# Kernel tuning notes

Measured on AMD Instinct MI355X. Metric: run time of the kernel, lower is better.

The kernel has to match this reference:

```python
import jax, jax.numpy as jnp
import numpy as np

E = 8          # num_experts
K = 2          # top_k
D = 1024       # hidden_size
I = 4096       # intermediate_size
AUX_COEF = 0.02


def setup_inputs() -> dict:
    key = jax.random.key(0)
    ks = jax.random.split(key, 5)
    x = jax.random.normal(ks[0], (4, 2048, D), dtype=jnp.float32)
    w_gate = jax.random.normal(ks[1], (E, D), dtype=jnp.float32) * 0.02   # router, nn.Linear weight [E, D]
    wg = jax.random.normal(ks[2], (E, D, I), dtype=jnp.float32) * 0.02    # gate_proj per expert
    wu = jax.random.normal(ks[3], (E, D, I), dtype=jnp.float32) * 0.02    # up_proj per expert
    wd = jax.random.normal(ks[4], (E, I, D), dtype=jnp.float32) * 0.02    # down_proj per expert
    return {"x": x, "w_gate": w_gate, "wg": wg, "wu": wu, "wd": wd}


def reference(x, w_gate, wg, wu, wd):
    B, T, Dm = x.shape
    xf = x.reshape(-1, Dm)                                   # [N, D]
    N = xf.shape[0]

    # 1) Router: softmax (in fp32) + top-k, renormalize top-k weights
    logits = xf @ w_gate.T                                   # [N, E]
    probs = jax.nn.softmax(logits.astype(jnp.float32), axis=-1)
    topk_w, topk_idx = jax.lax.top_k(probs, K)               # [N, K]
    topk_w = (topk_w / topk_w.sum(-1, keepdims=True)).astype(x.dtype)

    # Per-expert combine weight (zero when expert not selected) — math-equivalent
    # to the original gather/scatter-add loop but jit-friendly and vectorized.
    onehot = jax.nn.one_hot(topk_idx, E, dtype=x.dtype)      # [N, K, E]
    combine = jnp.einsum('nk,nke->ne', topk_w, onehot)       # [N, E]

    # 2) Experts: SwiGLU FFN, combined with routing weights
    out = jnp.zeros_like(xf)
    for e in range(E):  # fixed small loop over structurally distinct experts
        h = jax.nn.silu(xf @ wg[e]) * (xf @ wu[e])           # [N, I]
        out = out + combine[:, e:e + 1] * (h @ wd[e])        # [N, D]

    # 3) Load-balancing aux loss (Switch Transformer)
    f = onehot.sum((0, 1)).astype(jnp.float32) / (N * K)     # dispatch fraction per expert
    p = probs.mean(0)                                        # mean routing prob per expert
    aux_loss = AUX_COEF * E * jnp.sum(f * p)

    return out.reshape(B, T, Dm), aux_loss
```

## Files before the change

### kernel.cpp

```cpp
#include <hip/hip_runtime.h>
#include <hip/hip_bf16.h>
#include <cstdint>
#include <cstddef>

#define NE 8
#define TK 2
#define DM 1024
#define IM 4096
#define NT 8192
#define NS (NT*TK)
#define SCAP (NS+256)
#define MAXT 72

typedef __bf16 bf16_t;
typedef __bf16 bf16x8 __attribute__((ext_vector_type(8)));
typedef __bf16 bf16x4 __attribute__((ext_vector_type(4)));
typedef float f32x4 __attribute__((ext_vector_type(4)));

__device__ __forceinline__ void async_cp16(const bf16_t* g, bf16_t* l) {
  __builtin_amdgcn_global_load_lds(
      (__attribute__((address_space(1))) void*)(const_cast<bf16_t*>(g)),
      (__attribute__((address_space(3))) void*)(l), 16, 0, 0);
}

__global__ void transpose_cvt(const float* __restrict__ src, bf16_t* __restrict__ dst,
                              int R, int C) {
  __shared__ float t[32][33];
  int bx = blockIdx.x * 32, by = blockIdx.y * 32;
  size_t zb = (size_t)blockIdx.z * R * C;
  int tx = threadIdx.x, ty = threadIdx.y;
#pragma unroll
  for (int i = 0; i < 4; ++i)
    t[ty + i*8][tx] = src[zb + (size_t)(by + ty + i*8) * C + bx + tx];
  __syncthreads();
#pragma unroll
  for (int i = 0; i < 4; ++i)
    dst[zb + (size_t)(bx + ty + i*8) * R + by + tx] = (bf16_t)t[tx][ty + i*8];
}

__global__ void pack_gu(const float* __restrict__ wg, const float* __restrict__ wu,
                        bf16_t* __restrict__ Wgu) {
  __shared__ float t[32][33];
  int sel = blockIdx.z & 1, e = blockIdx.z >> 1;
  const float* src = sel ? wu : wg;
  size_t zb = (size_t)e * DM * IM;
  int bx = blockIdx.x * 32, by = blockIdx.y * 32;
  int tx = threadIdx.x, ty = threadIdx.y;
#pragma unroll
  for (int i = 0; i < 4; ++i)
    t[ty + i*8][tx] = src[zb + (size_t)(by + ty + i*8) * IM + bx + tx];
  __syncthreads();
#pragma unroll
  for (int i = 0; i < 4; ++i) {
    int icol = bx + ty + i*8;
    int p = ((icol >> 6) << 7) + (sel << 6) + (icol & 63);
    Wgu[((size_t)e * (2*IM) + p) * DM + by + tx] = (bf16_t)t[tx][ty + i*8];
  }
}

__global__ void router_kernel(const float* __restrict__ x, const float* __restrict__ wgate,
                              int* __restrict__ counts, float* __restrict__ prob_sum,
                              int* __restrict__ topk_idx, float* __restrict__ topk_w) {
  __shared__ float s_psum[NE];
  __shared__ int s_cnt[NE];
  int tid = threadIdx.x;
  if (tid < NE) { s_psum[tid] = 0.f; s_cnt[tid] = 0; }
  __syncthreads();
  int lane = tid & 63, wv = tid >> 6;
  for (int t = 0; t < 8; ++t) {
    int n = blockIdx.x * 32 + wv * 8 + t;
    float acc[NE];
#pragma unroll
    for (int e = 0; e < NE; ++e) acc[e] = 0.f;
#pragma unroll
    for (int j = 0; j < 16; ++j) {
      int d = j * 64 + lane;
      float xv = x[(size_t)n * DM + d];
#pragma unroll
      for (int e = 0; e < NE; ++e) acc[e] += xv * wgate[e * DM + d];
    }
#pragma unroll
    for (int e = 0; e < NE; ++e) {
#pragma unroll
      for (int off = 32; off > 0; off >>= 1) acc[e] += __shfl_xor(acc[e], off);
    }
    if (lane == 0) {
      float mx = acc[0];
#pragma unroll
      for (int e = 1; e < NE; ++e) mx = fmaxf(mx, acc[e]);
      float p[NE], s = 0.f;
#pragma unroll
      for (int e = 0; e < NE; ++e) { p[e] = __expf(acc[e] - mx); s += p[e]; }
      float inv = 1.f / s;
#pragma unroll
      for (int e = 0; e < NE; ++e) p[e] *= inv;
      int i0 = 0;
      for (int e = 1; e < NE; ++e) if (p[e] > p[i0]) i0 = e;
      int i1 = (i0 == 0) ? 1 : 0;
      for (int e = 0; e < NE; ++e) if (e != i0 && p[e] > p[i1]) i1 = e;
      float rs = 1.f / (p[i0] + p[i1]);
      topk_idx[n * 2 + 0] = i0; topk_idx[n * 2 + 1] = i1;
      topk_w[n * 2 + 0] = p[i0] * rs; topk_w[n * 2 + 1] = p[i1] * rs;
      atomicAdd(&s_cnt[i0], 1); atomicAdd(&s_cnt[i1], 1);
#pragma unroll
      for (int e = 0; e < NE; ++e) atomicAdd(&s_psum[e], p[e]);
    }
  }
  __syncthreads();
  if (tid < NE) { atomicAdd(&counts[tid], s_cnt[tid]); atomicAdd(&prob_sum[tid], s_psum[tid]); }
}

__global__ void scan_aux(const int* __restrict__ counts, const float* __restrict__ prob_sum,
                         int* __restrict__ offsets, int* __restrict__ cursors,
                         float* __restrict__ aux_out, int* __restrict__ tl_m0,
                         int* __restrict__ tl_e, int* __restrict__ tl_rows,
                         int* __restrict__ n_tiles) {
  if (threadIdx.x == 0) {
    int off = 0;
    float aux = 0.f;
    int t = 0;
    for (int e = 0; e < NE; ++e) {
      offsets[e] = off; cursors[e] = off;
      int c = counts[e];
      float f = (float)c * (1.f / (float)NS);
      float p = prob_sum[e] * (1.f / (float)NT);
      aux += f * p;
      for (int m = 0; m * 256 < c && t < MAXT; ++m, ++t) {
        tl_m0[t] = off + m * 256;
        tl_e[t] = e;
        tl_rows[t] = min(256, c - m * 256);
      }
      off += c;
    }
    offsets[NE] = off;
    *n_tiles = t;
    *aux_out = 0.02f * 8.f * aux;
  }
}

__global__ void gather_kernel(const float* __restrict__ x, const int* __restrict__ topk_idx,
                              const float* __restrict__ topk_w, int* __restrict__ cursors,
                              int* __restrict__ slot_token, float* __restrict__ slot_w,
                              int* __restrict__ pair_slot, bf16_t* __restrict__ Xg) {
  int lane = threadIdx.x & 63, wv = threadIdx.x >> 6;
  int pair = blockIdx.x * 4 + wv;
  int n = pair >> 1, k = pair & 1;
  int e = topk_idx[n * 2 + k];
  int slot = 0;
  if (lane == 0) slot = atomicAdd(&cursors[e], 1);
  slot = __shfl(slot, 0);
  if (lane == 0) {
    slot_token[slot] = n; slot_w[slot] = topk_w[n * 2 + k];
    pair_slot[pair] = slot;
  }
#pragma unroll
  for (int j = 0; j < 4; ++j) {
    int d4 = j * 256 + lane * 4;
    float4 v = *(const float4*)(x + (size_t)n * DM + d4);
    bf16x4 o;
    o[0] = (bf16_t)v.x; o[1] = (bf16_t)v.y; o[2] = (bf16_t)v.z; o[3] = (bf16_t)v.w;
    *(bf16x4*)(Xg + (size_t)slot * DM + d4) = o;
  }
}

#define MFMA16 __builtin_amdgcn_mfma_f32_16x16x32_bf16
#define SBAR  __builtin_amdgcn_s_barrier
#define SCHED __builtin_amdgcn_sched_barrier
#define PRIO  __builtin_amdgcn_s_setprio

template<int NTK, int KSTR, int BROWS, bool SWIGLU>
__global__ __launch_bounds__(512, 2) void moe_gemm(
    const bf16_t* __restrict__ A, const bf16_t* __restrict__ Bw,
    bf16_t* __restrict__ O,
    const int* __restrict__ tl_m0, const int* __restrict__ tl_e,
    const int* __restrict__ tl_rows, const int* __restrict__ n_tiles) {
  int ty = blockIdx.y;
  if (ty >= *n_tiles) return;
  int m0 = tl_m0[ty];
  int e  = tl_e[ty];
  int rows = tl_rows[ty];
  int nt = blockIdx.x;

  __shared__ bf16_t lds[2][4][128 * 64];

  int tid = threadIdx.x, lane = tid & 63, wv = tid >> 6;
  int fm = lane & 15, fq = lane >> 4;
  int wm = wv >> 2, wn = wv & 3;

  const bf16_t* Ab = A + (size_t)m0 * KSTR;
  const bf16_t* Bb = Bw + ((size_t)e * BROWS + (size_t)nt * 256) * KSTR;

  int sr = tid >> 3;
  int sgc = ((tid & 7) ^ (sr & 7)) << 3;
  int sldo = tid * 8;

#define STG(LDST, GBASE, COL) do {                                         \
    const bf16_t* _g = (GBASE);                                            \
    async_cp16(_g + (size_t)sr * KSTR + (COL) + sgc, (LDST) + sldo);       \
    async_cp16(_g + (size_t)(sr + 64) * KSTR + (COL) + sgc, (LDST) + sldo + 4096); \
  } while (0)

  int offA[4][2], offB[2][2];
#pragma unroll
  for (int m = 0; m < 4; ++m) {
    int r = m * 32 + wm * 16 + fm;
#pragma unroll
    for (int ks = 0; ks < 2; ++ks)
      offA[m][ks] = r * 64 + (((ks * 4 + fq) ^ (r & 7)) << 3);
  }
#pragma unroll
  for (int jh = 0; jh < 2; ++jh) {
    int r = jh * 64 + wn * 16 + fm;
#pragma unroll
    for (int ks = 0; ks < 2; ++ks)
      offB[jh][ks] = r * 64 + (((ks * 4 + fq) ^ (r & 7)) << 3);
  }

  f32x4 acc[8][4];
#pragma unroll
  for (int i = 0; i < 8; ++i)
#pragma unroll
    for (int j = 0; j < 4; ++j) acc[i][j] = (f32x4){0.f, 0.f, 0.f, 0.f};

  STG(lds[0][0], Ab, 0);
  STG(lds[0][2], Bb, 0);
  STG(lds[0][3], Bb + (size_t)128 * KSTR, 0);
  STG(lds[0][1], Ab + (size_t)128 * KSTR, 0);
  STG(lds[1][0], Ab, 64);
  STG(lds[1][2], Bb, 64);
  STG(lds[1][3], Bb + (size_t)128 * KSTR, 64);
  asm volatile("s_waitcnt vmcnt(6)");
  SBAR();
  SCHED(0);

  bf16x8 af[4][2], b0f[2][2], b1f[2][2];
#pragma unroll
  for (int j = 0; j < 2; ++j) {
    b0f[j][0] = *(const bf16x8*)(lds[0][2] + offB[j][0]);
    b0f[j][1] = *(const bf16x8*)(lds[0][2] + offB[j][1]);
  }
#pragma unroll
  for (int m = 0; m < 4; ++m) {
    af[m][0] = *(const bf16x8*)(lds[0][0] + offA[m][0]);
    af[m][1] = *(const bf16x8*)(lds[0][0] + offA[m][1]);
  }
  SCHED(0);

#pragma unroll 1
  for (int t = 0; t < NTK; ++t) {
    const int buf = t & 1;
    const bf16_t* LA1 = lds[buf][1];
    const bf16_t* LB1 = lds[buf][3];
    const bf16_t* NA0 = lds[buf ^ 1][0];
    const bf16_t* NB0 = lds[buf ^ 1][2];
    if (t + 1 < NTK) STG(lds[buf ^ 1][1], Ab + (size_t)128 * KSTR, (t + 1) * 64);
#pragma unroll
    for (int j = 0; j < 2; ++j) {
      b1f[j][0] = *(const bf16x8*)(LB1 + offB[j][0]);
      b1f[j][1] = *(const bf16x8*)(LB1 + offB[j][1]);
    }
    SCHED(0);
    asm volatile("s_waitcnt lgkmcnt(4)");
    SBAR();
    SCHED(0);
    PRIO(1);
#pragma unroll
    for (int m = 0; m < 4; ++m)
#pragma unroll
      for (int j = 0; j < 2; ++j) {
        acc[m][j] = MFMA16(af[m][0], b0f[j][0], acc[m][j], 0, 0, 0);
        acc[m][j] = MFMA16(af[m][1], b0f[j][1], acc[m][j], 0, 0, 0);
      }
    PRIO(0);
    SCHED(0);
    if (t + 2 < NTK) STG(lds[buf][0], Ab, (t + 2) * 64);
    SCHED(0);
    asm volatile("s_waitcnt lgkmcnt(0)");
    SBAR();
    SCHED(0);
    PRIO(1);
#pragma unroll
    for (int m = 0; m < 4; ++m)
#pragma unroll
      for (int j = 0; j < 2; ++j) {
        acc[m][2 + j] = MFMA16(af[m][0], b1f[j][0], acc[m][2 + j], 0, 0, 0);
        acc[m][2 + j] = MFMA16(af[m][1], b1f[j][1], acc[m][2 + j], 0, 0, 0);
      }
    PRIO(0);
    SCHED(0);
#pragma unroll
    for (int m = 0; m < 4; ++m) {
      af[m][0] = *(const bf16x8*)(LA1 + offA[m][0]);
      af[m][1] = *(const bf16x8*)(LA1 + offA[m][1]);
    }
    SCHED(0);
    if (t + 2 < NTK) STG(lds[buf][2], Bb, (t + 2) * 64);
    SCHED(0);
    asm volatile("s_waitcnt lgkmcnt(0)");
    SBAR();
    SCHED(0);
    PRIO(1);
#pragma unroll
    for (int m = 0; m < 4; ++m)
#pragma unroll
      for (int j = 0; j < 2; ++j) {
        acc[4 + m][j] = MFMA16(af[m][0], b0f[j][0], acc[4 + m][j], 0, 0, 0);
        acc[4 + m][j] = MFMA16(af[m][1], b0f[j][1], acc[4 + m][j], 0, 0, 0);
      }
    PRIO(0);
    SCHED(0);
    if (t + 2 < NTK) STG(lds[buf][3], Bb + (size_t)128 * KSTR, (t + 2) * 64);
    SCHED(0);
    if (t < NTK - 2)       { asm volatile("s_waitcnt vmcnt(6)"); }
    else if (t == NTK - 2) { asm volatile("s_waitcnt vmcnt(0)"); }
    SBAR();
    SCHED(0);
    if (t + 1 < NTK) {
#pragma unroll
      for (int j = 0; j < 2; ++j) {
        b0f[j][0] = *(const bf16x8*)(NB0 + offB[j][0]);
        b0f[j][1] = *(const bf16x8*)(NB0 + offB[j][1]);
      }
    }
    SCHED(0);
    PRIO(1);
#pragma unroll
    for (int m = 0; m < 4; ++m)
#pragma unroll
      for (int j = 0; j < 2; ++j) {
        acc[4 + m][2 + j] = MFMA16(af[m][0], b1f[j][0], acc[4 + m][2 + j], 0, 0, 0);
        acc[4 + m][2 + j] = MFMA16(af[m][1], b1f[j][1], acc[4 + m][2 + j], 0, 0, 0);
      }
    PRIO(0);
    SCHED(0);
    if (t + 1 < NTK) {
#pragma unroll
      for (int m = 0; m < 4; ++m) {
        af[m][0] = *(const bf16x8*)(NA0 + offA[m][0]);
        af[m][1] = *(const bf16x8*)(NA0 + offA[m][1]);
      }
    }
    SCHED(0);
  }
#undef STG

#pragma unroll
  for (int i = 0; i < 8; ++i) {
    int lr = i * 32 + wm * 16 + fq * 4;
#pragma unroll
    for (int rr = 0; rr < 4; ++rr) {
      if (lr + rr < rows) {
        if constexpr (SWIGLU) {
          bf16_t* hp = O + (size_t)(m0 + lr + rr) * IM + nt * 128 + wn * 16 + fm;
          float g0 = acc[i][0][rr], u0 = acc[i][1][rr];
          hp[0] = (bf16_t)(g0 * __builtin_amdgcn_rcpf(1.f + __expf(-g0)) * u0);
          float g1 = acc[i][2][rr], u1 = acc[i][3][rr];
          hp[64] = (bf16_t)(g1 * __builtin_amdgcn_rcpf(1.f + __expf(-g1)) * u1);
        } else {
          bf16_t* yp = O + (size_t)(m0 + lr + rr) * DM + nt * 256 + wn * 16 + fm;
          yp[0]   = (bf16_t)acc[i][0][rr];
          yp[64]  = (bf16_t)acc[i][1][rr];
          yp[128] = (bf16_t)acc[i][2][rr];
          yp[192] = (bf16_t)acc[i][3][rr];
        }
      }
    }
  }
}

__global__ void combine_kernel(const bf16_t* __restrict__ Y, const int* __restrict__ pair_slot,
                               const float* __restrict__ topk_w, float* __restrict__ out) {
  int n = blockIdx.x;
  int t = threadIdx.x;
  int s0 = pair_slot[n * 2 + 0], s1 = pair_slot[n * 2 + 1];
  float w0 = topk_w[n * 2 + 0], w1 = topk_w[n * 2 + 1];
  bf16x4 y0 = *(const bf16x4*)(Y + (size_t)s0 * DM + t * 4);
  bf16x4 y1 = *(const bf16x4*)(Y + (size_t)s1 * DM + t * 4);
  float4 o;
  o.x = w0 * (float)y0[0] + w1 * (float)y1[0];
  o.y = w0 * (float)y0[1] + w1 * (float)y1[1];
  o.z = w0 * (float)y0[2] + w1 * (float)y1[2];
  o.w = w0 * (float)y0[3] + w1 * (float)y1[3];
  *(float4*)(out + (size_t)n * DM + t * 4) = o;
}

static constexpr size_t OFF_TL    = 256;
static constexpr size_t OFF_TLE   = OFF_TL  + (size_t)MAXT * 4;
static constexpr size_t OFF_TLR   = OFF_TLE + (size_t)MAXT * 4;
static constexpr size_t OFF_NTL   = OFF_TLR + (size_t)MAXT * 4;
static constexpr size_t OFF_TOPKI = 1536;
static constexpr size_t OFF_TOPKW = OFF_TOPKI + (size_t)NT * 2 * 4;
static constexpr size_t OFF_STOK  = OFF_TOPKW + (size_t)NT * 2 * 4;
static constexpr size_t OFF_SW    = OFF_STOK + (size_t)NS * 4;
static constexpr size_t OFF_PSLOT = OFF_SW + (size_t)NS * 4;
static constexpr size_t OFF_XG    = OFF_PSLOT + (size_t)NS * 4;
static constexpr size_t OFF_H     = OFF_XG + (size_t)SCAP * DM * 2;
static constexpr size_t OFF_WGU   = OFF_H + (size_t)SCAP * IM * 2;
static constexpr size_t OFF_WDT   = OFF_WGU + (size_t)NE * 2 * IM * DM * 2;

extern "C" void kernel_launch(void* const* d_in, const int* in_sizes, int n_in,
                              void* d_out, int out_size, void* d_ws, size_t ws_size,
                              hipStream_t stream) {
  const float* x      = (const float*)d_in[0];
  const float* w_gate = (const float*)d_in[1];
  const float* wg     = (const float*)d_in[2];
  const float* wu     = (const float*)d_in[3];
  const float* wd     = (const float*)d_in[4];
  float* out = (float*)d_out;

  char* ws = (char*)d_ws;
  int*   counts   = (int*)(ws + 0);
  int*   cursors  = (int*)(ws + 32);
  int*   offsets  = (int*)(ws + 64);
  float* prob_sum = (float*)(ws + 128);
  int*   tl_m0    = (int*)(ws + OFF_TL);
  int*   tl_e     = (int*)(ws + OFF_TLE);
  int*   tl_rows  = (int*)(ws + OFF_TLR);
  int*   n_tiles  = (int*)(ws + OFF_NTL);
  int*   topk_idx = (int*)(ws + OFF_TOPKI);
  float* topk_w   = (float*)(ws + OFF_TOPKW);
  int*   slot_tok = (int*)(ws + OFF_STOK);
  float* slot_w   = (float*)(ws + OFF_SW);
  int*   pair_slot= (int*)(ws + OFF_PSLOT);
  bf16_t* Xg  = (bf16_t*)(ws + OFF_XG);
  bf16_t* Yb  = Xg;
  bf16_t* Hb  = (bf16_t*)(ws + OFF_H);
  bf16_t* Wgu = (bf16_t*)(ws + OFF_WGU);
  bf16_t* Wdt = (bf16_t*)(ws + OFF_WDT);

  hipMemsetAsync(ws, 0, 256, stream);

  pack_gu<<<dim3(IM / 32, DM / 32, NE * 2), dim3(32, 8), 0, stream>>>(wg, wu, Wgu);
  transpose_cvt<<<dim3(DM / 32, IM / 32, NE), dim3(32, 8), 0, stream>>>(wd, Wdt, IM, DM);

  router_kernel<<<NT / 32, 256, 0, stream>>>(x, w_gate, counts, prob_sum, topk_idx, topk_w);
  scan_aux<<<1, 64, 0, stream>>>(counts, prob_sum, offsets, cursors, out + (out_size - 1),
                                 tl_m0, tl_e, tl_rows, n_tiles);
  gather_kernel<<<NS / 4, 256, 0, stream>>>(x, topk_idx, topk_w, cursors, slot_tok, slot_w,
                                            pair_slot, Xg);

  moe_gemm<DM / 64, DM, 2 * IM, true><<<dim3(32, MAXT), 512, 0, stream>>>(
      Xg, Wgu, Hb, tl_m0, tl_e, tl_rows, n_tiles);
  moe_gemm<IM / 64, IM, DM, false><<<dim3(4, MAXT), 512, 0, stream>>>(
      Hb, Wdt, Yb, tl_m0, tl_e, tl_rows, n_tiles);

  combine_kernel<<<NT, 256, 0, stream>>>(Yb, pair_slot, topk_w, out);
}
```

Measured before the change: 1.183 ms.

## Split-K the down-projection GEMM and precompute staging pointers

The down-projection GEMM is split along K into two halves over a third grid dimension. Each half writes fp32 partial results into a buffer that reuses the gate/up weight workspace, and the combine kernel sums the two partials before applying the routing weights. This doubles the block count of the down GEMM, which previously had only 4 N-tiles per M-tile and so kept few CUs busy. The global staging addresses are also precomputed as incrementing pointers, and barriers are moved ahead of the LDS waitcnt. The cost is extra fp32 traffic for the partials and a wider combine read.

```diff
diff --git a/kernel.cpp b/kernel.cpp
--- a/kernel.cpp
+++ b/kernel.cpp
@@ -168,10 +168,10 @@
 #define SCHED __builtin_amdgcn_sched_barrier
 #define PRIO  __builtin_amdgcn_s_setprio
 
-template<int NTK, int KSTR, int BROWS, bool SWIGLU>
+template<int NTK, int KSTR, int BROWS, bool SWIGLU, int KSPLIT>
 __global__ __launch_bounds__(512, 2) void moe_gemm(
     const bf16_t* __restrict__ A, const bf16_t* __restrict__ Bw,
-    bf16_t* __restrict__ O,
+    void* __restrict__ O,
     const int* __restrict__ tl_m0, const int* __restrict__ tl_e,
     const int* __restrict__ tl_rows, const int* __restrict__ n_tiles) {
   int ty = blockIdx.y;
@@ -180,6 +180,8 @@
   int e  = tl_e[ty];
   int rows = tl_rows[ty];
   int nt = blockIdx.x;
+  int kh = (KSPLIT > 1) ? (int)blockIdx.z : 0;
+  constexpr int KC = NTK * 64;
 
   __shared__ bf16_t lds[2][4][128 * 64];
 
@@ -187,8 +189,8 @@
   int fm = lane & 15, fq = lane >> 4;
   int wm = wv >> 2, wn = wv & 3;
 
-  const bf16_t* Ab = A + (size_t)m0 * KSTR;
-  const bf16_t* Bb = Bw + ((size_t)e * BROWS + (size_t)nt * 256) * KSTR;
+  const bf16_t* Ab = A + (size_t)m0 * KSTR + kh * KC;
+  const bf16_t* Bb = Bw + ((size_t)e * BROWS + (size_t)nt * 256) * KSTR + kh * KC;
 
   int sr = tid >> 3;
   int sgc = ((tid & 7) ^ (sr & 7)) << 3;
@@ -198,6 +200,10 @@
     const bf16_t* _g = (GBASE);                                            \
     async_cp16(_g + (size_t)sr * KSTR + (COL) + sgc, (LDST) + sldo);       \
     async_cp16(_g + (size_t)(sr + 64) * KSTR + (COL) + sgc, (LDST) + sldo + 4096); \
+  } while (0)
+#define STG2(LDST, PLO, PHI) do {                                          \
+    async_cp16((PLO), (LDST) + sldo);                                      \
+    async_cp16((PHI), (LDST) + sldo + 4096);                               \
   } while (0)
 
   int offA[4][2], offB[2][2];
@@ -229,6 +235,16 @@
   STG(lds[1][0], Ab, 64);
   STG(lds[1][2], Bb, 64);
   STG(lds[1][3], Bb + (size_t)128 * KSTR, 64);
+
+  const bf16_t* qA1a = Ab + (size_t)(128 + sr) * KSTR + sgc + 64;
+  const bf16_t* qA1b = Ab + (size_t)(192 + sr) * KSTR + sgc + 64;
+  const bf16_t* qA0a = Ab + (size_t)sr * KSTR + sgc + 128;
+  const bf16_t* qA0b = Ab + (size_t)(64 + sr) * KSTR + sgc + 128;
+  const bf16_t* qB0a = Bb + (size_t)sr * KSTR + sgc + 128;
+  const bf16_t* qB0b = Bb + (size_t)(64 + sr) * KSTR + sgc + 128;
+  const bf16_t* qB1a = Bb + (size_t)(128 + sr) * KSTR + sgc + 128;
+  const bf16_t* qB1b = Bb + (size_t)(192 + sr) * KSTR + sgc + 128;
+
   asm volatile("s_waitcnt vmcnt(6)");
   SBAR();
   SCHED(0);
@@ -253,7 +269,7 @@
     const bf16_t* LB1 = lds[buf][3];
     const bf16_t* NA0 = lds[buf ^ 1][0];
     const bf16_t* NB0 = lds[buf ^ 1][2];
-    if (t + 1 < NTK) STG(lds[buf ^ 1][1], Ab + (size_t)128 * KSTR, (t + 1) * 64);
+    if (t + 1 < NTK) STG2(lds[buf ^ 1][1], qA1a, qA1b);
 #pragma unroll
     for (int j = 0; j < 2; ++j) {
       b1f[j][0] = *(const bf16x8*)(LB1 + offB[j][0]);
@@ -273,10 +289,10 @@
       }
     PRIO(0);
     SCHED(0);
-    if (t + 2 < NTK) STG(lds[buf][0], Ab, (t + 2) * 64);
-    SCHED(0);
+    if (t + 2 < NTK) STG2(lds[buf][0], qA0a, qA0b);
+    SCHED(0);
+    SBAR();
     asm volatile("s_waitcnt lgkmcnt(0)");
-    SBAR();
     SCHED(0);
     PRIO(1);
 #pragma unroll
@@ -294,10 +310,10 @@
       af[m][1] = *(const bf16x8*)(LA1 + offA[m][1]);
     }
     SCHED(0);
-    if (t + 2 < NTK) STG(lds[buf][2], Bb, (t + 2) * 64);
-    SCHED(0);
+    if (t + 2 < NTK) STG2(lds[buf][2], qB0a, qB0b);
+    SCHED(0);
+    SBAR();
     asm volatile("s_waitcnt lgkmcnt(0)");
-    SBAR();
     SCHED(0);
     PRIO(1);
 #pragma unroll
@@ -309,7 +325,7 @@
       }
     PRIO(0);
     SCHED(0);
-    if (t + 2 < NTK) STG(lds[buf][3], Bb + (size_t)128 * KSTR, (t + 2) * 64);
+    if (t + 2 < NTK) STG2(lds[buf][3], qB1a, qB1b);
     SCHED(0);
     if (t < NTK - 2)       { asm volatile("s_waitcnt vmcnt(6)"); }
     else if (t == NTK - 2) { asm volatile("s_waitcnt vmcnt(0)"); }
@@ -341,8 +357,11 @@
       }
     }
     SCHED(0);
+    qA1a += 64; qA1b += 64; qA0a += 64; qA0b += 64;
+    qB0a += 64; qB0b += 64; qB1a += 64; qB1b += 64;
   }
 #undef STG
+#undef STG2
 
 #pragma unroll
   for (int i = 0; i < 8; ++i) {
@@ -351,36 +370,40 @@
     for (int rr = 0; rr < 4; ++rr) {
       if (lr + rr < rows) {
         if constexpr (SWIGLU) {
-          bf16_t* hp = O + (size_t)(m0 + lr + rr) * IM + nt * 128 + wn * 16 + fm;
+          bf16_t* hp = (bf16_t*)O + (size_t)(m0 + lr + rr) * IM + nt * 128 + wn * 16 + fm;
           float g0 = acc[i][0][rr], u0 = acc[i][1][rr];
           hp[0] = (bf16_t)(g0 * __builtin_amdgcn_rcpf(1.f + __expf(-g0)) * u0);
           float g1 = acc[i][2][rr], u1 = acc[i][3][rr];
           hp[64] = (bf16_t)(g1 * __builtin_amdgcn_rcpf(1.f + __expf(-g1)) * u1);
         } else {
-          bf16_t* yp = O + (size_t)(m0 + lr + rr) * DM + nt * 256 + wn * 16 + fm;
-          yp[0]   = (bf16_t)acc[i][0][rr];
-          yp[64]  = (bf16_t)acc[i][1][rr];
-          yp[128] = (bf16_t)acc[i][2][rr];
-          yp[192] = (bf16_t)acc[i][3][rr];
+          float* yp = (float*)O + (size_t)kh * ((size_t)NS * DM)
+                      + (size_t)(m0 + lr + rr) * DM + nt * 256 + wn * 16 + fm;
+          yp[0]   = acc[i][0][rr];
+          yp[64]  = acc[i][1][rr];
+          yp[128] = acc[i][2][rr];
+          yp[192] = acc[i][3][rr];
         }
       }
     }
   }
 }
 
-__global__ void combine_kernel(const bf16_t* __restrict__ Y, const int* __restrict__ pair_slot,
+__global__ void combine_kernel(const float* __restrict__ Yp, const int* __restrict__ pair_slot,
                                const float* __restrict__ topk_w, float* __restrict__ out) {
   int n = blockIdx.x;
   int t = threadIdx.x;
   int s0 = pair_slot[n * 2 + 0], s1 = pair_slot[n * 2 + 1];
   float w0 = topk_w[n * 2 + 0], w1 = topk_w[n * 2 + 1];
-  bf16x4 y0 = *(const bf16x4*)(Y + (size_t)s0 * DM + t * 4);
-  bf16x4 y1 = *(const bf16x4*)(Y + (size_t)s1 * DM + t * 4);
+  const size_t half = (size_t)NS * DM;
+  float4 a0 = *(const float4*)(Yp + (size_t)s0 * DM + t * 4);
+  float4 a1 = *(const float4*)(Yp + half + (size_t)s0 * DM + t * 4);
+  float4 b0 = *(const float4*)(Yp + (size_t)s1 * DM + t * 4);
+  float4 b1 = *(const float4*)(Yp + half + (size_t)s1 * DM + t * 4);
   float4 o;
-  o.x = w0 * (float)y0[0] + w1 * (float)y1[0];
-  o.y = w0 * (float)y0[1] + w1 * (float)y1[1];
-  o.z = w0 * (float)y0[2] + w1 * (float)y1[2];
-  o.w = w0 * (float)y0[3] + w1 * (float)y1[3];
+  o.x = w0 * (a0.x + a1.x) + w1 * (b0.x + b1.x);
+  o.y = w0 * (a0.y + a1.y) + w1 * (b0.y + b1.y);
+  o.z = w0 * (a0.z + a1.z) + w1 * (b0.z + b1.z);
+  o.w = w0 * (a0.w + a1.w) + w1 * (b0.w + b1.w);
   *(float4*)(out + (size_t)n * DM + t * 4) = o;
 }
 
@@ -423,10 +446,10 @@
   float* slot_w   = (float*)(ws + OFF_SW);
   int*   pair_slot= (int*)(ws + OFF_PSLOT);
   bf16_t* Xg  = (bf16_t*)(ws + OFF_XG);
-  bf16_t* Yb  = Xg;
   bf16_t* Hb  = (bf16_t*)(ws + OFF_H);
   bf16_t* Wgu = (bf16_t*)(ws + OFF_WGU);
   bf16_t* Wdt = (bf16_t*)(ws + OFF_WDT);
+  float*  Yp  = (float*)(ws + OFF_WGU);
 
   hipMemsetAsync(ws, 0, 256, stream);
 
@@ -439,10 +462,10 @@
   gather_kernel<<<NS / 4, 256, 0, stream>>>(x, topk_idx, topk_w, cursors, slot_tok, slot_w,
                                             pair_slot, Xg);
 
-  moe_gemm<DM / 64, DM, 2 * IM, true><<<dim3(32, MAXT), 512, 0, stream>>>(
-      Xg, Wgu, Hb, tl_m0, tl_e, tl_rows, n_tiles);
-  moe_gemm<IM / 64, IM, DM, false><<<dim3(4, MAXT), 512, 0, stream>>>(
-      Hb, Wdt, Yb, tl_m0, tl_e, tl_rows, n_tiles);
-
-  combine_kernel<<<NT, 256, 0, stream>>>(Yb, pair_slot, topk_w, out);
-}
+  moe_gemm<DM / 64, DM, 2 * IM, true, 1><<<dim3(32, MAXT, 1), 512, 0, stream>>>(
+      Xg, Wgu, (void*)Hb, tl_m0, tl_e, tl_rows, n_tiles);
+  moe_gemm<IM / 128, IM, DM, false, 2><<<dim3(4, MAXT, 2), 512, 0, stream>>>(
+      Hb, Wdt, (void*)Yp, tl_m0, tl_e, tl_rows, n_tiles);
+
+  combine_kernel<<<NT, 256, 0, stream>>>(Yp, pair_slot, topk_w, out);
+}
```

Measured after the change: 1.167 ms. No clear change (-1.4%).
